# Kernel optimization log

Measured on AMD Instinct MI355X. Metric: run time of the kernel, lower is better.

Reference implementation:

```python
import jax, jax.numpy as jnp
import numpy as np

BLOCK = 64
CRIT_TH = 0.5
NEGL_TH = 0.01
TEMP = 1.0
EPS = 1e-6


def setup_inputs() -> dict:
    key = jax.random.key(0)
    kq, kk, kv = jax.random.split(key, 3)
    B, T, H, D = 1, 2048, 8, 64
    q = jax.random.normal(kq, (B, T, H, D), dtype=jnp.float32)
    k = jax.random.normal(kk, (B, T, H, D), dtype=jnp.float32)
    v = jax.random.normal(kv, (B, T, H, D), dtype=jnp.float32)
    return {"q": q, "k": k, "v": v}


def _classify_blocks(qb, kb, D):
    # qb: [B,nq,bs,H,D], kb: [B,nk,bs,H,D]
    q_rep = qb.mean(axis=2)  # [B,nq,H,D]
    k_rep = kb.mean(axis=2)  # [B,nk,H,D]
    bscores = jnp.einsum('bqhd,bkhd->bhqk', q_rep, k_rep) / np.float32(np.sqrt(D))
    ssm = jax.nn.softmax(bscores, axis=-1)
    var = jnp.var(ssm, axis=-1, ddof=1, keepdims=True)  # unbiased, matches torch .var()
    max_scores = bscores.max(axis=-1, keepdims=True)
    imp = var * jnp.maximum(max_scores - bscores.min(), EPS)
    imp_n = (imp - imp.min()) / (imp.max() - imp.min() + EPS)
    crit = imp_n >= CRIT_TH
    negl = imp_n <= NEGL_TH
    marg = (~crit) & (~negl)
    return crit, marg


def reference(q, k, v):
    B, T, H, D = q.shape
    S = k.shape[1]
    nq, nk = T // BLOCK, S // BLOCK  # T,S are multiples of BLOCK (no padding needed)
    dtype = q.dtype

    qb = q.reshape(B, nq, BLOCK, H, D)
    kb = k.reshape(B, nk, BLOCK, H, D)
    vb = v.reshape(B, nk, BLOCK, H, D)

    crit, marg = _classify_blocks(qb, kb, D)  # [B,H,nq,nk] bool
    critf = crit.astype(dtype)
    margf = marg.astype(dtype)

    # ---- exact (critical) blocks: per-block-pair softmax attention ----
    scale = np.float32(1.0 / (np.sqrt(D) * TEMP))
    scores = jnp.einsum('bqthd,bkshd->bhqkts', qb, kb) * scale  # [B,H,nq,nk,bs,bs]
    attn = jax.nn.softmax(scores.astype(jnp.float32), axis=-1).astype(dtype)
    attn_m = attn * critf[:, :, :, :, None, None]
    out_c = jnp.einsum('bhqkts,bkshd->bqthd', attn_m, vb)  # [B,nq,bs,H,D]
    w_c = jnp.einsum('bhqkts->bqth', attn_m)[..., None]    # [B,nq,bs,H,1]

    # ---- linear (marginal) blocks: ELU+1 feature-map attention ----
    qf = jax.nn.elu(qb / TEMP) + 1.0
    kf = jax.nn.elu(kb / TEMP) + 1.0
    kv = jnp.einsum('bkshd,bkshv->bkhdv', kf, vb)              # [B,nk,H,D,D]
    num = jnp.einsum('bqthd,bkhdv->bqkthv', qf, kv)            # [B,nq,nk,bs,H,D]
    k_sum = kf.sum(axis=2)                                     # [B,nk,H,D]
    den = jnp.einsum('bqthd,bkhd->bqkth', qf, k_sum) + EPS     # [B,nq,nk,bs,H]
    out_pair = num / den[..., None]
    out_l = jnp.einsum('bqkthd,bhqk->bqthd', out_pair, margf)
    w_l = jnp.einsum('bqkth,bhqk->bqth', den, margf)[..., None]

    out = (out_c + out_l) / (w_c + w_l + EPS)
    return out.reshape(B, T, H, D)
```

## Files before the change

### kernel.cpp

```cpp
#include <hip/hip_runtime.h>
#include <math.h>

namespace {
constexpr int H  = 8;
constexpr int D  = 64;
constexpr int NB = 32;
constexpr int BS = 64;
constexpr int QST = 68;
constexpr int KSPLIT = 8;
constexpr int KCH = NB / KSPLIT;
}
#define FEPS 1e-6f

typedef unsigned short u16;
typedef unsigned int   u32;
typedef __attribute__((ext_vector_type(8))) short bf16x8;
typedef __attribute__((ext_vector_type(4))) float floatx4;

__device__ __forceinline__ u32 f2bf(float x) {
  union { float f; u32 u; } v; v.f = x;
  return (v.u + 0x7FFFu + ((v.u >> 16) & 1u)) >> 16;
}
__device__ __forceinline__ u32 pk2(float a, float b) { return f2bf(a) | (f2bf(b) << 16); }
#define ELU1(x) ((x) > 0.f ? (x) + 1.f : expf(x))
#define SWZ(row, kblk) ((row)*64 + (((kblk) ^ ((row)&7))*8))

__global__ __launch_bounds__(256) void prep_kernel(const float* __restrict__ q,
                                                   const float* __restrict__ k,
                                                   const float* __restrict__ v,
                                                   u16* __restrict__ kvt16,
                                                   float* __restrict__ ksum,
                                                   double* __restrict__ qrep,
                                                   double* __restrict__ krep) {
  __shared__ float smem[3*BS*D];
  int bid = blockIdx.x;
  int tid = threadIdx.x;
  if (bid >= 256) {
    double* qred = (double*)smem;
    int r = bid - 256;
    int h = r >> 5, bi = r & 31;
    int d = tid & 63, quarter = tid >> 6;
    double s = 0.0;
    for (int t = quarter*16; t < quarter*16 + 16; ++t)
      s += (double)q[((bi*BS + t)*H + h)*D + d];
    qred[quarter*64 + d] = s;
    __syncthreads();
    if (tid < 64)
      qrep[r*D + tid] = (qred[tid] + qred[64+tid] + qred[128+tid] + qred[192+tid]) * (1.0/64.0);
    return;
  }
  float* kf   = smem;
  float* vv   = smem + BS*D;
  float* kraw = smem + 2*BS*D;
  int h = bid >> 5, ki = bid & 31;
  int sr = tid >> 2, cgp = tid & 3;
  const float4* kb = (const float4*)(k + ((ki*BS + sr)*H + h)*D);
  const float4* vb = (const float4*)(v + ((ki*BS + sr)*H + h)*D);
#pragma unroll
  for (int m = 0; m < 4; ++m) {
    float4 kk = kb[cgp*4 + m];
    float4 vx = vb[cgp*4 + m];
    int c = cgp*16 + m*4;
    *(float4*)&kraw[sr*D + c] = kk;
    kf[sr*D + c + 0] = ELU1(kk.x);
    kf[sr*D + c + 1] = ELU1(kk.y);
    kf[sr*D + c + 2] = ELU1(kk.z);
    kf[sr*D + c + 3] = ELU1(kk.w);
    *(float4*)&vv[sr*D + c] = vx;
  }
  __syncthreads();
  int c = tid & 63, dg = tid >> 6, d0 = dg*16;
  float acc[16];
#pragma unroll
  for (int j = 0; j < 16; ++j) acc[j] = 0.f;
#pragma unroll 4
  for (int s2 = 0; s2 < BS; ++s2) {
    float vval = vv[s2*D + c];
    const float4* kr = (const float4*)&kf[s2*D + d0];
    float4 a0 = kr[0], a1 = kr[1], a2 = kr[2], a3 = kr[3];
    acc[0]  += vval*a0.x; acc[1]  += vval*a0.y; acc[2]  += vval*a0.z; acc[3]  += vval*a0.w;
    acc[4]  += vval*a1.x; acc[5]  += vval*a1.y; acc[6]  += vval*a1.z; acc[7]  += vval*a1.w;
    acc[8]  += vval*a2.x; acc[9]  += vval*a2.y; acc[10] += vval*a2.z; acc[11] += vval*a2.w;
    acc[12] += vval*a3.x; acc[13] += vval*a3.y; acc[14] += vval*a3.z; acc[15] += vval*a3.w;
  }
  u16* op = kvt16 + (size_t)bid*4096 + c*64 + d0;
  uint4 P0, P1;
  P0.x = pk2(acc[0],acc[1]);   P0.y = pk2(acc[2],acc[3]);
  P0.z = pk2(acc[4],acc[5]);   P0.w = pk2(acc[6],acc[7]);
  P1.x = pk2(acc[8],acc[9]);   P1.y = pk2(acc[10],acc[11]);
  P1.z = pk2(acc[12],acc[13]); P1.w = pk2(acc[14],acc[15]);
  *(uint4*)(op + 0) = P0;
  *(uint4*)(op + 8) = P1;
  if (dg == 0) {
    float ks = 0.f;
    for (int s2 = 0; s2 < BS; ++s2) ks += kf[s2*D + c];
    ksum[bid*D + c] = ks;
    double m = 0.0;
    for (int s2 = 0; s2 < BS; ++s2) m += (double)kraw[s2*D + c];
    krep[bid*D + c] = m * (1.0/64.0);
  }
}

__global__ __launch_bounds__(256) void bscore_stats_kernel(const double* __restrict__ qrep,
                                                           const double* __restrict__ krep,
                                                           double* __restrict__ rowmin,
                                                           double* __restrict__ rowmax,
                                                           double* __restrict__ rowvar) {
  __shared__ double qs[8*64];
  __shared__ double ks[32*65];
  int b = blockIdx.x;
  int h = b >> 2;
  int r0 = b*8;
  int tid = threadIdx.x;
  for (int i = tid; i < 512; i += 256) qs[i] = qrep[(size_t)r0*64 + i];
  for (int i = tid; i < 2048; i += 256) ks[(i >> 6)*65 + (i & 63)] = krep[(size_t)h*2048 + i];
  __syncthreads();
  int lr = tid >> 5, ki = tid & 31;
  double s = 0.0;
  const double* qr = qs + lr*64;
  const double* kr = ks + ki*65;
#pragma unroll 16
  for (int d = 0; d < D; ++d) s += qr[d]*kr[d];
  double bs = s * 0.125;
  double rmax = bs, rmin = bs;
#pragma unroll
  for (int m = 1; m < 32; m <<= 1) {
    rmax = fmax(rmax, __shfl_xor(rmax, m, 64));
    rmin = fmin(rmin, __shfl_xor(rmin, m, 64));
  }
  double e = exp(bs - rmax);
  double S = e, S2 = e*e;
#pragma unroll
  for (int m = 1; m < 32; m <<= 1) {
    S  += __shfl_xor(S,  m, 64);
    S2 += __shfl_xor(S2, m, 64);
  }
  if (ki == 0) {
    double invS = 1.0 / S;
    double sp = S * invS;
    double mu = sp * (1.0/32.0);
    double var = (S2*invS*invS - 2.0*mu*sp + 32.0*mu*mu) * (1.0/31.0);
    rowmin[r0 + lr] = rmin;
    rowmax[r0 + lr] = rmax;
    rowvar[r0 + lr] = var;
  }
}

__global__ __launch_bounds__(256) void flags_kernel(const double* __restrict__ rowmin,
                                                    const double* __restrict__ rowmax,
                                                    const double* __restrict__ rowvar,
                                                    int* __restrict__ flags) {
  __shared__ double redA[4];
  __shared__ double redB[4];
  int tid = threadIdx.x;
  int lane = tid & 63, wid = tid >> 6;
  double x = rowmin[tid];
#pragma unroll
  for (int m = 1; m < 64; m <<= 1) x = fmin(x, __shfl_xor(x, m, 64));
  if (lane == 0) redA[wid] = x;
  __syncthreads();
  double gmin = fmin(fmin(redA[0], redA[1]), fmin(redA[2], redA[3]));
  double rng = rowmax[tid] - gmin;
  if (rng < 1e-6) rng = 1e-6;
  double imp = rowvar[tid] * rng;
  __syncthreads();
  double a = imp, b2 = imp;
#pragma unroll
  for (int m = 1; m < 64; m <<= 1) {
    a  = fmin(a,  __shfl_xor(a,  m, 64));
    b2 = fmax(b2, __shfl_xor(b2, m, 64));
  }
  if (lane == 0) { redA[wid] = a; redB[wid] = b2; }
  __syncthreads();
  double imin = fmin(fmin(redA[0], redA[1]), fmin(redA[2], redA[3]));
  double imax = fmax(fmax(redB[0], redB[1]), fmax(redB[2], redB[3]));
  double impn = (imp - imin) / (imax - imin + 1e-6);
  flags[tid] = (impn >= 0.5) ? 2 : ((impn <= 0.01) ? 0 : 1);
}

__global__ __launch_bounds__(256) void main_kernel(
    const float* __restrict__ q, const float* __restrict__ k, const float* __restrict__ v,
    const u16* __restrict__ kvt16, const float* __restrict__ ksum,
    const int* __restrict__ flags, float* __restrict__ pacc, float* __restrict__ pw) {
  __shared__ __align__(16) float smem[13056];
  int bid = blockIdx.x;
  int rowid = bid >> 3;
  int split = bid & (KSPLIT - 1);
  int h = rowid >> 5, qi = rowid & 31;
  int k0 = split * KCH;
  int tid = threadIdx.x;
  int row = tid >> 2, cgp = tid & 3, c0 = cgp*16;
  int lane = tid & 63;

  float* paccp = pacc + (size_t)bid * 4096;
  float* pwp   = pw   + (size_t)bid * 64;

  int flag = flags[rowid];
  if (flag == 0) {
    if (tid < 64) pwp[tid] = 0.f;
    return;
  }

  if (flag == 1) {
    u16*  qfb  = (u16*)smem;
    u16*  kvb  = (u16*)(smem + 2048);
    float* idens = smem + 6144;
    float* wsl   = smem + 6400;
    float* kslc  = smem + 6464;

    {
      const float4* kss = (const float4*)(ksum + (size_t)(h*NB + k0)*D);
      for (int i = tid; i < KCH*16; i += 256) ((float4*)kslc)[i] = kss[i];
    }
    float qf[16];
    {
      const float4* qp = (const float4*)(q + ((qi*BS + row)*H + h)*D + c0);
      float4 q0 = qp[0], q1 = qp[1], q2 = qp[2], q3 = qp[3];
      qf[0]=ELU1(q0.x); qf[1]=ELU1(q0.y); qf[2]=ELU1(q0.z); qf[3]=ELU1(q0.w);
      qf[4]=ELU1(q1.x); qf[5]=ELU1(q1.y); qf[6]=ELU1(q1.z); qf[7]=ELU1(q1.w);
      qf[8]=ELU1(q2.x); qf[9]=ELU1(q2.y); qf[10]=ELU1(q2.z); qf[11]=ELU1(q2.w);
      qf[12]=ELU1(q3.x); qf[13]=ELU1(q3.y); qf[14]=ELU1(q3.z); qf[15]=ELU1(q3.w);
      uint4 p0, p1;
      p0.x = pk2(qf[0],qf[1]);  p0.y = pk2(qf[2],qf[3]);
      p0.z = pk2(qf[4],qf[5]);  p0.w = pk2(qf[6],qf[7]);
      p1.x = pk2(qf[8],qf[9]);  p1.y = pk2(qf[10],qf[11]);
      p1.z = pk2(qf[12],qf[13]); p1.w = pk2(qf[14],qf[15]);
      *(uint4*)&qfb[SWZ(row, cgp*2)]     = p0;
      *(uint4*)&qfb[SWZ(row, cgp*2 + 1)] = p1;
    }
    const u16* kvbase = kvt16 + (size_t)(h*NB + k0)*4096 + (size_t)row*64 + c0;
    uint4 u0 = *(const uint4*)(kvbase + 0);
    uint4 u1 = *(const uint4*)(kvbase + 8);
    __syncthreads();
    {
      float wloc = 0.f;
      for (int kk = 0; kk < KCH; ++kk) {
        float pd = 0.f;
#pragma unroll
        for (int j = 0; j < 16; ++j) pd += qf[j] * kslc[kk*64 + c0 + j];
        pd += __shfl_xor(pd, 1, 64);
        pd += __shfl_xor(pd, 2, 64);
        float den = pd + FEPS;
        if (cgp == 0) idens[row*KCH + kk] = 1.0f / den;
        wloc += den;
      }
      if (cgp == 0) wsl[row] = wloc;
    }
    *(uint4*)&kvb[SWZ(row, cgp*2)]     = u0;
    *(uint4*)&kvb[SWZ(row, cgp*2 + 1)] = u1;

    int w = tid >> 6, m = lane & 15, quad = lane >> 4;
    bf16x8 aLo = *(const bf16x8*)&qfb[SWZ(w*16 + m, quad)];
    bf16x8 aHi = *(const bf16x8*)&qfb[SWZ(w*16 + m, 4 + quad)];
    int rbase = w*16 + quad*4;
    float acc[16];
#pragma unroll
    for (int j = 0; j < 16; ++j) acc[j] = 0.f;

    for (int kk = 0; kk < KCH; ++kk) {
      if (kk + 1 < KCH) {
        const u16* kvp = kvbase + (size_t)(kk+1)*4096;
        u0 = *(const uint4*)(kvp + 0);
        u1 = *(const uint4*)(kvp + 8);
      }
      __syncthreads();
      const u16* kb = kvb + (kk & 1)*4096;
      float i0 = idens[(rbase + 0)*KCH + kk];
      float i1 = idens[(rbase + 1)*KCH + kk];
      float i2 = idens[(rbase + 2)*KCH + kk];
      float i3 = idens[(rbase + 3)*KCH + kk];
      floatx4 zz = {0.f, 0.f, 0.f, 0.f};
#pragma unroll
      for (int t = 0; t < 4; ++t) {
        bf16x8 bLo = *(const bf16x8*)&kb[SWZ(t*16 + m, quad)];
        bf16x8 bHi = *(const bf16x8*)&kb[SWZ(t*16 + m, 4 + quad)];
        floatx4 c4 = __builtin_amdgcn_mfma_f32_16x16x32_bf16(aLo, bLo, zz, 0, 0, 0);
        c4 = __builtin_amdgcn_mfma_f32_16x16x32_bf16(aHi, bHi, c4, 0, 0, 0);
        acc[t*4+0] += c4[0]*i0;
        acc[t*4+1] += c4[1]*i1;
        acc[t*4+2] += c4[2]*i2;
        acc[t*4+3] += c4[3]*i3;
      }
      if (kk + 1 < KCH) {
        u16* kw = kvb + ((kk+1) & 1)*4096;
        *(uint4*)&kw[SWZ(row, cgp*2)]     = u0;
        *(uint4*)&kw[SWZ(row, cgp*2 + 1)] = u1;
      }
    }
#pragma unroll
    for (int r = 0; r < 4; ++r)
#pragma unroll
      for (int t = 0; t < 4; ++t)
        paccp[(rbase + r)*64 + t*16 + m] = acc[t*4 + r];
    if (tid < 64) pwp[tid] = wsl[tid];
    return;
  }

  float* bufA = smem;
  float* bufK = smem + 4352;
  float* bufV = smem + 8704;
  {
    const float4* qp = (const float4*)(q + ((qi*BS + row)*H + h)*D);
#pragma unroll
    for (int mm = 0; mm < 4; ++mm) {
      float4 qq = qp[cgp*4 + mm];
      int c = c0 + mm*4;
      bufA[row*QST + c + 0] = qq.x*0.125f;
      bufA[row*QST + c + 1] = qq.y*0.125f;
      bufA[row*QST + c + 2] = qq.z*0.125f;
      bufA[row*QST + c + 3] = qq.w*0.125f;
    }
  }
  float4 kreg[4], vreg[4];
  {
    const float4* kp = (const float4*)(k + ((k0*BS + row)*H + h)*D);
    const float4* vp = (const float4*)(v + ((k0*BS + row)*H + h)*D);
#pragma unroll
    for (int mm = 0; mm < 4; ++mm) { kreg[mm] = kp[cgp*4 + mm]; vreg[mm] = vp[cgp*4 + mm]; }
  }
  float acc[16];
#pragma unroll
  for (int j = 0; j < 16; ++j) acc[j] = 0.f;
  float wsum = 0.f;

#pragma unroll 1
  for (int kk = 0; kk < KCH; ++kk) {
#pragma unroll
    for (int mm = 0; mm < 4; ++mm) {
      int c = c0 + mm*4;
      bufK[(c+0)*QST + row] = kreg[mm].x;
      bufK[(c+1)*QST + row] = kreg[mm].y;
      bufK[(c+2)*QST + row] = kreg[mm].z;
      bufK[(c+3)*QST + row] = kreg[mm].w;
      *(float4*)&bufV[row*QST + c] = vreg[mm];
    }
    __syncthreads();
    if (kk + 1 < KCH) {
      int ki1 = k0 + kk + 1;
      const float4* kp = (const float4*)(k + ((ki1*BS + row)*H + h)*D);
      const float4* vp = (const float4*)(v + ((ki1*BS + row)*H + h)*D);
#pragma unroll
      for (int mm = 0; mm < 4; ++mm) { kreg[mm] = kp[cgp*4 + mm]; vreg[mm] = vp[cgp*4 + mm]; }
    }
    float sc[16];
#pragma unroll
    for (int j = 0; j < 16; ++j) sc[j] = 0.f;
#pragma unroll 4
    for (int d4 = 0; d4 < 16; ++d4) {
      float4 a4 = *(const float4*)&bufA[row*QST + d4*4];
      float av[4] = {a4.x, a4.y, a4.z, a4.w};
#pragma unroll
      for (int x = 0; x < 4; ++x) {
        const float4* br = (const float4*)&bufK[(d4*4 + x)*QST + c0];
        float4 b0 = br[0], b1 = br[1], b2 = br[2], b3 = br[3];
        float a = av[x];
        sc[0]  += a*b0.x; sc[1]  += a*b0.y; sc[2]  += a*b0.z; sc[3]  += a*b0.w;
        sc[4]  += a*b1.x; sc[5]  += a*b1.y; sc[6]  += a*b1.z; sc[7]  += a*b1.w;
        sc[8]  += a*b2.x; sc[9]  += a*b2.y; sc[10] += a*b2.z; sc[11] += a*b2.w;
        sc[12] += a*b3.x; sc[13] += a*b3.y; sc[14] += a*b3.z; sc[15] += a*b3.w;
      }
    }
    float mx = sc[0];
#pragma unroll
    for (int j = 1; j < 16; ++j) mx = fmaxf(mx, sc[j]);
    mx = fmaxf(mx, __shfl_xor(mx, 1, 64));
    mx = fmaxf(mx, __shfl_xor(mx, 2, 64));
    float es = 0.f;
    float p[16];
#pragma unroll
    for (int j = 0; j < 16; ++j) { p[j] = expf(sc[j] - mx); es += p[j]; }
    es += __shfl_xor(es, 1, 64);
    es += __shfl_xor(es, 2, 64);
    float inv = 1.0f / es;
#pragma unroll
    for (int j = 0; j < 16; ++j) p[j] *= inv;
    wsum += es * inv;
#pragma unroll 1
    for (int g = 0; g < 4; ++g) {
      int src = (lane & ~3) | g;
#pragma unroll
      for (int jj = 0; jj < 16; ++jj) {
        float pv = __shfl(p[jj], src, 64);
        const float4* vr = (const float4*)&bufV[(g*16 + jj)*QST + c0];
        float4 a0 = vr[0], a1 = vr[1], a2 = vr[2], a3 = vr[3];
        acc[0]  += pv*a0.x; acc[1]  += pv*a0.y; acc[2]  += pv*a0.z; acc[3]  += pv*a0.w;
        acc[4]  += pv*a1.x; acc[5]  += pv*a1.y; acc[6]  += pv*a1.z; acc[7]  += pv*a1.w;
        acc[8]  += pv*a2.x; acc[9]  += pv*a2.y; acc[10] += pv*a2.z; acc[11] += pv*a2.w;
        acc[12] += pv*a3.x; acc[13] += pv*a3.y; acc[14] += pv*a3.z; acc[15] += pv*a3.w;
      }
    }
    __syncthreads();
  }
  float* pp = paccp + row*64 + c0;
  *(float4*)(pp + 0)  = make_float4(acc[0],  acc[1],  acc[2],  acc[3]);
  *(float4*)(pp + 4)  = make_float4(acc[4],  acc[5],  acc[6],  acc[7]);
  *(float4*)(pp + 8)  = make_float4(acc[8],  acc[9],  acc[10], acc[11]);
  *(float4*)(pp + 12) = make_float4(acc[12], acc[13], acc[14], acc[15]);
  if (cgp == 0) pwp[row] = wsum;
}

__global__ __launch_bounds__(256) void combine_kernel(const float* __restrict__ pacc,
                                                      const float* __restrict__ pw,
                                                      float* __restrict__ out) {
  int rowid = blockIdx.x;
  int h = rowid >> 5, qi = rowid & 31;
  int tid = threadIdx.x;
  int row = tid >> 2, c0 = (tid & 3)*16;
  float w = 0.f;
  const float* pwb = pw + (size_t)rowid * KSPLIT * 64 + row;
#pragma unroll
  for (int s = 0; s < KSPLIT; ++s) w += pwb[s*64];
  float* op = out + ((qi*BS + row)*H + h)*D + c0;
  if (w == 0.f) {
    float4 z = make_float4(0.f, 0.f, 0.f, 0.f);
    ((float4*)op)[0] = z; ((float4*)op)[1] = z; ((float4*)op)[2] = z; ((float4*)op)[3] = z;
    return;
  }
  floatx4 s0 = {0,0,0,0}, s1 = {0,0,0,0}, s2 = {0,0,0,0}, s3 = {0,0,0,0};
  const float* base = pacc + (size_t)rowid * KSPLIT * 4096 + row*64 + c0;
#pragma unroll
  for (int s = 0; s < KSPLIT; ++s) {
    const floatx4* p4 = (const floatx4*)(base + (size_t)s*4096);
    s0 += p4[0]; s1 += p4[1]; s2 += p4[2]; s3 += p4[3];
  }
  float wd = 1.0f / (w + FEPS);
  ((float4*)op)[0] = make_float4(s0[0]*wd, s0[1]*wd, s0[2]*wd, s0[3]*wd);
  ((float4*)op)[1] = make_float4(s1[0]*wd, s1[1]*wd, s1[2]*wd, s1[3]*wd);
  ((float4*)op)[2] = make_float4(s2[0]*wd, s2[1]*wd, s2[2]*wd, s2[3]*wd);
  ((float4*)op)[3] = make_float4(s3[0]*wd, s3[1]*wd, s3[2]*wd, s3[3]*wd);
}

extern "C" void kernel_launch(void* const* d_in, const int* in_sizes, int n_in,
                              void* d_out, int out_size, void* d_ws, size_t ws_size,
                              hipStream_t stream) {
  const float* q = (const float*)d_in[0];
  const float* k = (const float*)d_in[1];
  const float* v = (const float*)d_in[2];
  float* out = (float*)d_out;
  char* ws = (char*)d_ws;
  u16*    kvw  = (u16*)   (ws + 0);
  float*  ksw  = (float*) (ws + 2097152);
  double* krep = (double*)(ws + 2162688);
  double* qrep = (double*)(ws + 2293760);
  double* rmn  = (double*)(ws + 2424832);
  double* rmx  = (double*)(ws + 2426880);
  double* rvr  = (double*)(ws + 2428928);
  int*    flg  = (int*)   (ws + 2430976);
  float*  pacc = (float*) (ws + 4194304);
  float*  pw   = (float*) (ws + 4194304 + 33554432);

  prep_kernel<<<512, 256, 0, stream>>>(q, k, v, kvw, ksw, qrep, krep);
  bscore_stats_kernel<<<32, 256, 0, stream>>>(qrep, krep, rmn, rmx, rvr);
  flags_kernel<<<1, 256, 0, stream>>>(rmn, rmx, rvr, flg);
  main_kernel<<<256*KSPLIT, 256, 0, stream>>>(q, k, v, kvw, ksw, flg, pacc, pw);
  combine_kernel<<<256, 256, 0, stream>>>(pacc, pw, out);
}
```

Measured before the change: 103.5 us.

## Use split-bf16 MFMA for exact critical-block attention and halve K splits

Replaces the scalar fp32 QK^T and PV loops in the critical-block path with MFMA bf16 matrix instructions. Each fp32 operand is split into hi and lo bf16 parts and three cross products are summed to keep close to fp32 accuracy. Q, K, V and P are staged in swizzled LDS, with V stored transposed. KSPLIT drops from 8 to 4, which halves the partial-result buffers and the combine traffic but gives each block twice as many key chunks and fewer blocks overall. The risk is some accuracy loss from the dropped lo*lo term, plus more LDS use per block.

```diff
diff --git a/kernel.cpp b/kernel.cpp
--- a/kernel.cpp
+++ b/kernel.cpp
@@ -6,8 +6,7 @@
 constexpr int D  = 64;
 constexpr int NB = 32;
 constexpr int BS = 64;
-constexpr int QST = 68;
-constexpr int KSPLIT = 8;
+constexpr int KSPLIT = 4;
 constexpr int KCH = NB / KSPLIT;
 }
 #define FEPS 1e-6f
@@ -22,8 +21,41 @@
   return (v.u + 0x7FFFu + ((v.u >> 16) & 1u)) >> 16;
 }
 __device__ __forceinline__ u32 pk2(float a, float b) { return f2bf(a) | (f2bf(b) << 16); }
+__device__ __forceinline__ u32 split_pack(float x) {
+  u32 h = f2bf(x);
+  union { u32 u; float f; } hf; hf.u = h << 16;
+  u32 l = f2bf(x - hf.f);
+  return h | (l << 16);
+}
+__device__ __forceinline__ void split2(float a, float b, u32& hw, u32& lw) {
+  u32 ha = f2bf(a), hb = f2bf(b);
+  union { u32 u; float f; } fa, fb; fa.u = ha << 16; fb.u = hb << 16;
+  hw = ha | (hb << 16);
+  lw = f2bf(a - fa.f) | (f2bf(b - fb.f) << 16);
+}
+__device__ __forceinline__ bf16x8 plane_lo(uint4 a, uint4 b) {
+  union { u32 u[4]; bf16x8 v; } r;
+  r.u[0] = __builtin_amdgcn_perm(a.y, a.x, 0x05040100u);
+  r.u[1] = __builtin_amdgcn_perm(a.w, a.z, 0x05040100u);
+  r.u[2] = __builtin_amdgcn_perm(b.y, b.x, 0x05040100u);
+  r.u[3] = __builtin_amdgcn_perm(b.w, b.z, 0x05040100u);
+  return r.v;
+}
+__device__ __forceinline__ bf16x8 plane_hi(uint4 a, uint4 b) {
+  union { u32 u[4]; bf16x8 v; } r;
+  r.u[0] = __builtin_amdgcn_perm(a.y, a.x, 0x07060302u);
+  r.u[1] = __builtin_amdgcn_perm(a.w, a.z, 0x07060302u);
+  r.u[2] = __builtin_amdgcn_perm(b.y, b.x, 0x07060302u);
+  r.u[3] = __builtin_amdgcn_perm(b.w, b.z, 0x07060302u);
+  return r.v;
+}
 #define ELU1(x) ((x) > 0.f ? (x) + 1.f : expf(x))
 #define SWZ(row, kblk) ((row)*64 + (((kblk) ^ ((row)&7))*8))
+#define SPLIT8(F0, F1, UH, UL, SCALE) do { \
+  split2((F0).x*(SCALE), (F0).y*(SCALE), (UH).x, (UL).x); \
+  split2((F0).z*(SCALE), (F0).w*(SCALE), (UH).y, (UL).y); \
+  split2((F1).x*(SCALE), (F1).y*(SCALE), (UH).z, (UL).z); \
+  split2((F1).z*(SCALE), (F1).w*(SCALE), (UH).w, (UL).w); } while(0)
 
 __global__ __launch_bounds__(256) void prep_kernel(const float* __restrict__ q,
                                                    const float* __restrict__ k,
@@ -182,15 +214,16 @@
     const float* __restrict__ q, const float* __restrict__ k, const float* __restrict__ v,
     const u16* __restrict__ kvt16, const float* __restrict__ ksum,
     const int* __restrict__ flags, float* __restrict__ pacc, float* __restrict__ pw) {
-  __shared__ __align__(16) float smem[13056];
+  __shared__ __align__(16) float smem[16384];
   int bid = blockIdx.x;
-  int rowid = bid >> 3;
+  int rowid = bid >> 2;
   int split = bid & (KSPLIT - 1);
   int h = rowid >> 5, qi = rowid & 31;
   int k0 = split * KCH;
   int tid = threadIdx.x;
   int row = tid >> 2, cgp = tid & 3, c0 = cgp*16;
   int lane = tid & 63;
+  int w = tid >> 6, m = lane & 15, q4 = lane >> 4;
 
   float* paccp = pacc + (size_t)bid * 4096;
   float* pwp   = pw   + (size_t)bid * 64;
@@ -205,8 +238,8 @@
     u16*  qfb  = (u16*)smem;
     u16*  kvb  = (u16*)(smem + 2048);
     float* idens = smem + 6144;
-    float* wsl   = smem + 6400;
-    float* kslc  = smem + 6464;
+    float* wsl   = smem + 6656;
+    float* kslc  = smem + 6720;
 
     {
       const float4* kss = (const float4*)(ksum + (size_t)(h*NB + k0)*D);
@@ -249,10 +282,9 @@
     *(uint4*)&kvb[SWZ(row, cgp*2)]     = u0;
     *(uint4*)&kvb[SWZ(row, cgp*2 + 1)] = u1;
 
-    int w = tid >> 6, m = lane & 15, quad = lane >> 4;
-    bf16x8 aLo = *(const bf16x8*)&qfb[SWZ(w*16 + m, quad)];
-    bf16x8 aHi = *(const bf16x8*)&qfb[SWZ(w*16 + m, 4 + quad)];
-    int rbase = w*16 + quad*4;
+    bf16x8 aLo = *(const bf16x8*)&qfb[SWZ(w*16 + m, q4)];
+    bf16x8 aHi = *(const bf16x8*)&qfb[SWZ(w*16 + m, 4 + q4)];
+    int rbase = w*16 + q4*4;
     float acc[16];
 #pragma unroll
     for (int j = 0; j < 16; ++j) acc[j] = 0.f;
@@ -272,8 +304,8 @@
       floatx4 zz = {0.f, 0.f, 0.f, 0.f};
 #pragma unroll
       for (int t = 0; t < 4; ++t) {
-        bf16x8 bLo = *(const bf16x8*)&kb[SWZ(t*16 + m, quad)];
-        bf16x8 bHi = *(const bf16x8*)&kb[SWZ(t*16 + m, 4 + quad)];
+        bf16x8 bLo = *(const bf16x8*)&kb[SWZ(t*16 + m, q4)];
+        bf16x8 bHi = *(const bf16x8*)&kb[SWZ(t*16 + m, 4 + q4)];
         floatx4 c4 = __builtin_amdgcn_mfma_f32_16x16x32_bf16(aLo, bLo, zz, 0, 0, 0);
         c4 = __builtin_amdgcn_mfma_f32_16x16x32_bf16(aHi, bHi, c4, 0, 0, 0);
         acc[t*4+0] += c4[0]*i0;
@@ -296,107 +328,158 @@
     return;
   }
 
-  float* bufA = smem;
-  float* bufK = smem + 4352;
-  float* bufV = smem + 8704;
+  u16* qhi = (u16*)smem;
+  u16* qlo = (u16*)(smem + 2048);
+  u16* khi = (u16*)(smem + 4096);
+  u16* klo = (u16*)(smem + 6144);
+  u32* vt32 = (u32*)(smem + 8192);
+  u32* p32  = (u32*)(smem + 12288);
+
   {
-    const float4* qp = (const float4*)(q + ((qi*BS + row)*H + h)*D);
-#pragma unroll
-    for (int mm = 0; mm < 4; ++mm) {
-      float4 qq = qp[cgp*4 + mm];
-      int c = c0 + mm*4;
-      bufA[row*QST + c + 0] = qq.x*0.125f;
-      bufA[row*QST + c + 1] = qq.y*0.125f;
-      bufA[row*QST + c + 2] = qq.z*0.125f;
-      bufA[row*QST + c + 3] = qq.w*0.125f;
-    }
+    const float4* qp = (const float4*)(q + ((qi*BS + row)*H + h)*D + c0);
+    float4 q0 = qp[0], q1 = qp[1], q2 = qp[2], q3 = qp[3];
+    uint4 UH, UL;
+    SPLIT8(q0, q1, UH, UL, 0.125f);
+    *(uint4*)&qhi[SWZ(row, cgp*2)] = UH;
+    *(uint4*)&qlo[SWZ(row, cgp*2)] = UL;
+    SPLIT8(q2, q3, UH, UL, 0.125f);
+    *(uint4*)&qhi[SWZ(row, cgp*2 + 1)] = UH;
+    *(uint4*)&qlo[SWZ(row, cgp*2 + 1)] = UL;
   }
   float4 kreg[4], vreg[4];
   {
-    const float4* kp = (const float4*)(k + ((k0*BS + row)*H + h)*D);
-    const float4* vp = (const float4*)(v + ((k0*BS + row)*H + h)*D);
-#pragma unroll
-    for (int mm = 0; mm < 4; ++mm) { kreg[mm] = kp[cgp*4 + mm]; vreg[mm] = vp[cgp*4 + mm]; }
-  }
+    const float4* kp = (const float4*)(k + ((k0*BS + row)*H + h)*D + c0);
+    const float4* vp = (const float4*)(v + ((k0*BS + row)*H + h)*D + c0);
+#pragma unroll
+    for (int mm = 0; mm < 4; ++mm) { kreg[mm] = kp[mm]; vreg[mm] = vp[mm]; }
+  }
+  __syncthreads();
+  bf16x8 qh0 = *(const bf16x8*)&qhi[SWZ(w*16 + m, q4)];
+  bf16x8 qh1 = *(const bf16x8*)&qhi[SWZ(w*16 + m, 4 + q4)];
+  bf16x8 ql0 = *(const bf16x8*)&qlo[SWZ(w*16 + m, q4)];
+  bf16x8 ql1 = *(const bf16x8*)&qlo[SWZ(w*16 + m, 4 + q4)];
+
+  int rbase = w*16 + q4*4;
+  int ibase = (w*16 + m)*64;
   float acc[16];
 #pragma unroll
   for (int j = 0; j < 16; ++j) acc[j] = 0.f;
-  float wsum = 0.f;
+  float wsum4[4] = {0.f, 0.f, 0.f, 0.f};
 
 #pragma unroll 1
   for (int kk = 0; kk < KCH; ++kk) {
-#pragma unroll
-    for (int mm = 0; mm < 4; ++mm) {
-      int c = c0 + mm*4;
-      bufK[(c+0)*QST + row] = kreg[mm].x;
-      bufK[(c+1)*QST + row] = kreg[mm].y;
-      bufK[(c+2)*QST + row] = kreg[mm].z;
-      bufK[(c+3)*QST + row] = kreg[mm].w;
-      *(float4*)&bufV[row*QST + c] = vreg[mm];
+    {
+      uint4 UH, UL;
+      SPLIT8(kreg[0], kreg[1], UH, UL, 1.0f);
+      *(uint4*)&khi[SWZ(row, cgp*2)] = UH;
+      *(uint4*)&klo[SWZ(row, cgp*2)] = UL;
+      SPLIT8(kreg[2], kreg[3], UH, UL, 1.0f);
+      *(uint4*)&khi[SWZ(row, cgp*2 + 1)] = UH;
+      *(uint4*)&klo[SWZ(row, cgp*2 + 1)] = UL;
+#pragma unroll
+      for (int mm = 0; mm < 4; ++mm) {
+        float4 vx = vreg[mm];
+        int dd = c0 + mm*4;
+        vt32[(dd+0)*64 + ((((row>>3)) ^ ((dd+0)&7))*8) + (row&7)] = split_pack(vx.x);
+        vt32[(dd+1)*64 + ((((row>>3)) ^ ((dd+1)&7))*8) + (row&7)] = split_pack(vx.y);
+        vt32[(dd+2)*64 + ((((row>>3)) ^ ((dd+2)&7))*8) + (row&7)] = split_pack(vx.z);
+        vt32[(dd+3)*64 + ((((row>>3)) ^ ((dd+3)&7))*8) + (row&7)] = split_pack(vx.w);
+      }
     }
     __syncthreads();
     if (kk + 1 < KCH) {
       int ki1 = k0 + kk + 1;
-      const float4* kp = (const float4*)(k + ((ki1*BS + row)*H + h)*D);
-      const float4* vp = (const float4*)(v + ((ki1*BS + row)*H + h)*D);
-#pragma unroll
-      for (int mm = 0; mm < 4; ++mm) { kreg[mm] = kp[cgp*4 + mm]; vreg[mm] = vp[cgp*4 + mm]; }
+      const float4* kp = (const float4*)(k + ((ki1*BS + row)*H + h)*D + c0);
+      const float4* vp = (const float4*)(v + ((ki1*BS + row)*H + h)*D + c0);
+#pragma unroll
+      for (int mm = 0; mm < 4; ++mm) { kreg[mm] = kp[mm]; vreg[mm] = vp[mm]; }
     }
     float sc[16];
 #pragma unroll
-    for (int j = 0; j < 16; ++j) sc[j] = 0.f;
-#pragma unroll 4
-    for (int d4 = 0; d4 < 16; ++d4) {
-      float4 a4 = *(const float4*)&bufA[row*QST + d4*4];
-      float av[4] = {a4.x, a4.y, a4.z, a4.w};
-#pragma unroll
-      for (int x = 0; x < 4; ++x) {
-        const float4* br = (const float4*)&bufK[(d4*4 + x)*QST + c0];
-        float4 b0 = br[0], b1 = br[1], b2 = br[2], b3 = br[3];
-        float a = av[x];
-        sc[0]  += a*b0.x; sc[1]  += a*b0.y; sc[2]  += a*b0.z; sc[3]  += a*b0.w;
-        sc[4]  += a*b1.x; sc[5]  += a*b1.y; sc[6]  += a*b1.z; sc[7]  += a*b1.w;
-        sc[8]  += a*b2.x; sc[9]  += a*b2.y; sc[10] += a*b2.z; sc[11] += a*b2.w;
-        sc[12] += a*b3.x; sc[13] += a*b3.y; sc[14] += a*b3.z; sc[15] += a*b3.w;
+    for (int t = 0; t < 4; ++t) {
+      bf16x8 bh0 = *(const bf16x8*)&khi[SWZ(t*16 + m, q4)];
+      bf16x8 bh1 = *(const bf16x8*)&khi[SWZ(t*16 + m, 4 + q4)];
+      bf16x8 bl0 = *(const bf16x8*)&klo[SWZ(t*16 + m, q4)];
+      bf16x8 bl1 = *(const bf16x8*)&klo[SWZ(t*16 + m, 4 + q4)];
+      floatx4 c4 = {0.f, 0.f, 0.f, 0.f};
+      c4 = __builtin_amdgcn_mfma_f32_16x16x32_bf16(qh0, bh0, c4, 0, 0, 0);
+      c4 = __builtin_amdgcn_mfma_f32_16x16x32_bf16(qh1, bh1, c4, 0, 0, 0);
+      c4 = __builtin_amdgcn_mfma_f32_16x16x32_bf16(qh0, bl0, c4, 0, 0, 0);
+      c4 = __builtin_amdgcn_mfma_f32_16x16x32_bf16(qh1, bl1, c4, 0, 0, 0);
+      c4 = __builtin_amdgcn_mfma_f32_16x16x32_bf16(ql0, bh0, c4, 0, 0, 0);
+      c4 = __builtin_amdgcn_mfma_f32_16x16x32_bf16(ql1, bh1, c4, 0, 0, 0);
+      sc[t*4+0] = c4[0]; sc[t*4+1] = c4[1]; sc[t*4+2] = c4[2]; sc[t*4+3] = c4[3];
+    }
+    float inv4[4];
+#pragma unroll
+    for (int r = 0; r < 4; ++r) {
+      float mxr = fmaxf(fmaxf(sc[r], sc[4+r]), fmaxf(sc[8+r], sc[12+r]));
+      mxr = fmaxf(mxr, __shfl_xor(mxr, 1, 64));
+      mxr = fmaxf(mxr, __shfl_xor(mxr, 2, 64));
+      mxr = fmaxf(mxr, __shfl_xor(mxr, 4, 64));
+      mxr = fmaxf(mxr, __shfl_xor(mxr, 8, 64));
+      float e0 = expf(sc[r] - mxr),  e1 = expf(sc[4+r] - mxr);
+      float e2 = expf(sc[8+r] - mxr), e3 = expf(sc[12+r] - mxr);
+      sc[r] = e0; sc[4+r] = e1; sc[8+r] = e2; sc[12+r] = e3;
+      float es = e0 + e1 + e2 + e3;
+      es += __shfl_xor(es, 1, 64);
+      es += __shfl_xor(es, 2, 64);
+      es += __shfl_xor(es, 4, 64);
+      es += __shfl_xor(es, 8, 64);
+      float iv = 1.0f / es;
+      wsum4[r] += es * iv;
+      inv4[r] = iv;
+    }
+#pragma unroll
+    for (int t = 0; t < 4; ++t) {
+#pragma unroll
+      for (int r = 0; r < 4; ++r) {
+        int i2 = rbase + r;
+        int jg = t*2 + (m >> 3);
+        p32[i2*64 + ((jg ^ (i2 & 7))*8) + (m & 7)] = split_pack(sc[t*4+r]);
       }
     }
-    float mx = sc[0];
-#pragma unroll
-    for (int j = 1; j < 16; ++j) mx = fmaxf(mx, sc[j]);
-    mx = fmaxf(mx, __shfl_xor(mx, 1, 64));
-    mx = fmaxf(mx, __shfl_xor(mx, 2, 64));
-    float es = 0.f;
-    float p[16];
-#pragma unroll
-    for (int j = 0; j < 16; ++j) { p[j] = expf(sc[j] - mx); es += p[j]; }
-    es += __shfl_xor(es, 1, 64);
-    es += __shfl_xor(es, 2, 64);
-    float inv = 1.0f / es;
-#pragma unroll
-    for (int j = 0; j < 16; ++j) p[j] *= inv;
-    wsum += es * inv;
-#pragma unroll 1
-    for (int g = 0; g < 4; ++g) {
-      int src = (lane & ~3) | g;
-#pragma unroll
-      for (int jj = 0; jj < 16; ++jj) {
-        float pv = __shfl(p[jj], src, 64);
-        const float4* vr = (const float4*)&bufV[(g*16 + jj)*QST + c0];
-        float4 a0 = vr[0], a1 = vr[1], a2 = vr[2], a3 = vr[3];
-        acc[0]  += pv*a0.x; acc[1]  += pv*a0.y; acc[2]  += pv*a0.z; acc[3]  += pv*a0.w;
-        acc[4]  += pv*a1.x; acc[5]  += pv*a1.y; acc[6]  += pv*a1.z; acc[7]  += pv*a1.w;
-        acc[8]  += pv*a2.x; acc[9]  += pv*a2.y; acc[10] += pv*a2.z; acc[11] += pv*a2.w;
-        acc[12] += pv*a3.x; acc[13] += pv*a3.y; acc[14] += pv*a3.z; acc[15] += pv*a3.w;
-      }
+    asm volatile("s_waitcnt lgkmcnt(0)" ::: "memory");
+    uint4 a00 = *(const uint4*)&p32[ibase + ((q4 ^ (m & 7))*8)];
+    uint4 a01 = *(const uint4*)&p32[ibase + ((q4 ^ (m & 7))*8) + 4];
+    uint4 a10 = *(const uint4*)&p32[ibase + (((4 + q4) ^ (m & 7))*8)];
+    uint4 a11 = *(const uint4*)&p32[ibase + (((4 + q4) ^ (m & 7))*8) + 4];
+    bf16x8 aPh0 = plane_lo(a00, a01), aPl0 = plane_hi(a00, a01);
+    bf16x8 aPh1 = plane_lo(a10, a11), aPl1 = plane_hi(a10, a11);
+#pragma unroll
+    for (int t = 0; t < 4; ++t) {
+      int dm = t*16 + m;
+      int vb0 = dm*64 + ((q4 ^ (m & 7))*8);
+      int vb1 = dm*64 + (((4 + q4) ^ (m & 7))*8);
+      uint4 v00 = *(const uint4*)&vt32[vb0];
+      uint4 v01 = *(const uint4*)&vt32[vb0 + 4];
+      uint4 v10 = *(const uint4*)&vt32[vb1];
+      uint4 v11 = *(const uint4*)&vt32[vb1 + 4];
+      bf16x8 vh0 = plane_lo(v00, v01), vl0 = plane_hi(v00, v01);
+      bf16x8 vh1 = plane_lo(v10, v11), vl1 = plane_hi(v10, v11);
+      floatx4 c4 = {0.f, 0.f, 0.f, 0.f};
+      c4 = __builtin_amdgcn_mfma_f32_16x16x32_bf16(aPh0, vh0, c4, 0, 0, 0);
+      c4 = __builtin_amdgcn_mfma_f32_16x16x32_bf16(aPh1, vh1, c4, 0, 0, 0);
+      c4 = __builtin_amdgcn_mfma_f32_16x16x32_bf16(aPh0, vl0, c4, 0, 0, 0);
+      c4 = __builtin_amdgcn_mfma_f32_16x16x32_bf16(aPh1, vl1, c4, 0, 0, 0);
+      c4 = __builtin_amdgcn_mfma_f32_16x16x32_bf16(aPl0, vh0, c4, 0, 0, 0);
+      c4 = __builtin_amdgcn_mfma_f32_16x16x32_bf16(aPl1, vh1, c4, 0, 0, 0);
+      acc[t*4+0] += c4[0]*inv4[0];
+      acc[t*4+1] += c4[1]*inv4[1];
+      acc[t*4+2] += c4[2]*inv4[2];
+      acc[t*4+3] += c4[3]*inv4[3];
     }
     __syncthreads();
   }
-  float* pp = paccp + row*64 + c0;
-  *(float4*)(pp + 0)  = make_float4(acc[0],  acc[1],  acc[2],  acc[3]);
-  *(float4*)(pp + 4)  = make_float4(acc[4],  acc[5],  acc[6],  acc[7]);
-  *(float4*)(pp + 8)  = make_float4(acc[8],  acc[9],  acc[10], acc[11]);
-  *(float4*)(pp + 12) = make_float4(acc[12], acc[13], acc[14], acc[15]);
-  if (cgp == 0) pwp[row] = wsum;
+#pragma unroll
+  for (int r = 0; r < 4; ++r)
+#pragma unroll
+    for (int t = 0; t < 4; ++t)
+      paccp[(rbase + r)*64 + t*16 + m] = acc[t*4 + r];
+  if (m == 0) {
+#pragma unroll
+    for (int r = 0; r < 4; ++r) pwp[rbase + r] = wsum4[r];
+  }
 }
 
 __global__ __launch_bounds__(256) void combine_kernel(const float* __restrict__ pacc,
@@ -447,7 +530,7 @@
   double* rvr  = (double*)(ws + 2428928);
   int*    flg  = (int*)   (ws + 2430976);
   float*  pacc = (float*) (ws + 4194304);
-  float*  pw   = (float*) (ws + 4194304 + 33554432);
+  float*  pw   = (float*) (ws + 4194304 + 16777216);
 
   prep_kernel<<<512, 256, 0, stream>>>(q, k, v, kvw, ksw, qrep, krep);
   bscore_stats_kernel<<<32, 256, 0, stream>>>(qrep, krep, rmn, rmx, rvr);
```

Result: faster. 99.41 us (-4.0%).
